# Kernel optimization log

Measured on AMD Instinct MI355X. Metric: run time of the kernel, lower is better.

Reference implementation:

```python
import jax, jax.numpy as jnp
import numpy as np
from jax import lax

NUM_CLASSES = 91
C_FEAT = 2048
HF = WF = 16          # backbone feature map size (512px image / stride 32)
STRIDE = 32           # anchor stride, as in source generate_base_anchors
N_ANCHOR_TYPES = 9
NMS_THR = 0.5
K_ROIS = 100          # fixed proposal count after NMS (padded, jit-safe)
SPATIAL_SCALE = 1.0 / 16.0
POOL = 7
SR = 2                # sampling ratio (source uses adaptive -1; fixed here)


def conv2d(x, w, b, pad):
    y = lax.conv_general_dilated(x, w, (1, 1), pad,
                                 dimension_numbers=('NCHW', 'OIHW', 'NCHW'))
    return y + b[None, :, None, None]


def setup_inputs():
    key = jax.random.key(0)
    ks = jax.random.split(key, 16)
    f32 = jnp.float32
    def w(k, shape, s=0.01):
        return jax.random.normal(k, shape, f32) * s
    z = lambda n: jnp.zeros((n,), f32)
    D = C_FEAT * POOL * POOL  # 100352
    return dict(
        x=jax.random.normal(ks[0], (1, C_FEAT, HF, WF), f32),
        rpn_w=w(ks[1], (512, C_FEAT, 3, 3)), rpn_b=z(512),
        cls_w=w(ks[2], (18, 512, 1, 1)), cls_b=z(18),
        bbox_w=w(ks[3], (36, 512, 1, 1)), bbox_b=z(36),
        fc1c_w=w(ks[4], (D, 4096)), fc1c_b=z(4096),
        fc2c_w=w(ks[5], (4096, NUM_CLASSES)), fc2c_b=z(NUM_CLASSES),
        fc1b_w=w(ks[6], (D, 4096)), fc1b_b=z(4096),
        fc2b_w=w(ks[7], (4096, 4)), fc2b_b=z(4),
        m1_w=w(ks[8], (256, C_FEAT, 3, 3)), m1_b=z(256),
        mt_w=w(ks[9], (256, 256, 2, 2)), mt_b=z(256),  # ConvT weight [C_in,C_out,kh,kw]
        m2_w=w(ks[10], (1, 256, 1, 1)), m2_b=z(1),
    )


def _anchors(hf, wf):
    scales = jnp.array([8.0, 16.0, 32.0])
    ratios = jnp.array([0.5, 1.0, 2.0])
    ws = (scales[:, None] * jnp.sqrt(ratios)[None, :]).reshape(-1)  # scale-major, 9
    hs = (scales[:, None] / jnp.sqrt(ratios)[None, :]).reshape(-1)
    base = jnp.stack([-ws / 2, -hs / 2, ws / 2, hs / 2], axis=1)    # [9,4]
    sy, sx = jnp.meshgrid(jnp.arange(hf) * STRIDE, jnp.arange(wf) * STRIDE, indexing='ij')
    shifts = jnp.stack([sx, sy, sx, sy], -1).reshape(-1, 4).astype(jnp.float32)  # [HW,4]
    return (base[:, None, :] + shifts[None, :, :]).reshape(-1, 4)   # [9*HW,4] anchor-type major


def _decode(a, d):
    wa = a[:, 2] - a[:, 0]
    ha = a[:, 3] - a[:, 1]
    cx = a[:, 0] + 0.5 * wa
    cy = a[:, 1] + 0.5 * ha
    px = cx + d[:, 0] * wa
    py = cy + d[:, 1] * ha
    pw = jnp.exp(d[:, 2]) * wa
    ph = jnp.exp(d[:, 3]) * ha
    return jnp.stack([px - 0.5 * pw, py - 0.5 * ph, px + 0.5 * pw, py + 0.5 * ph], 1)


def _nms_topk(boxes, scores, thr, k):
    n = boxes.shape[0]
    order = jnp.argsort(-scores)
    b = boxes[order]
    s = scores[order]
    area = (b[:, 2] - b[:, 0]) * (b[:, 3] - b[:, 1])
    xx1 = jnp.maximum(b[:, None, 0], b[None, :, 0])
    yy1 = jnp.maximum(b[:, None, 1], b[None, :, 1])
    xx2 = jnp.minimum(b[:, None, 2], b[None, :, 2])
    yy2 = jnp.minimum(b[:, None, 3], b[None, :, 3])
    inter = jnp.clip(xx2 - xx1, 0) * jnp.clip(yy2 - yy1, 0)
    iou = inter / (area[:, None] + area[None, :] - inter + 1e-9)
    j = jnp.arange(n)
    def body(i, keep):
        sup = keep[i] & (iou[i] > thr) & (j > i)
        return keep & ~sup
    keep = lax.fori_loop(0, n, body, jnp.ones((n,), bool))
    masked = jnp.where(keep, s, -jnp.inf)
    vals, pos = lax.top_k(masked, k)
    valid = jnp.isfinite(vals)
    fb = jnp.where(valid[:, None], b[pos], 0.0)
    fs = jnp.where(valid, vals, 0.0)
    return fb, fs


def _roi_align(feat, boxes):
    # feat: [C,H,W]; boxes: [K,4] in image coords
    C, H, W = feat.shape
    r = boxes * SPATIAL_SCALE
    S = POOL * SR  # 14 sample points per side
    t = (jnp.arange(S, dtype=feat.dtype) + 0.5) / S
    gx = jnp.clip(r[:, 0:1] + t[None, :] * (r[:, 2:3] - r[:, 0:1]), 0.0, W - 1.0)
    gy = jnp.clip(r[:, 1:2] + t[None, :] * (r[:, 3:4] - r[:, 1:2]), 0.0, H - 1.0)
    x0 = jnp.floor(gx); y0 = jnp.floor(gy)
    lx = gx - x0; ly = gy - y0
    x0i = x0.astype(jnp.int32); y0i = y0.astype(jnp.int32)
    x1i = jnp.minimum(x0i + 1, W - 1); y1i = jnp.minimum(y0i + 1, H - 1)
    flat = feat.reshape(C, H * W)
    def g(yi, xi):  # yi:[K,S] row coords, xi:[K,S] col coords -> [C,K,S,S]
        idx = yi[:, :, None] * W + xi[:, None, :]
        return flat[:, idx]
    lyb = ly[:, :, None]; lxb = lx[:, None, :]
    v = ((1 - lyb) * (1 - lxb) * g(y0i, x0i)
         + (1 - lyb) * lxb * g(y0i, x1i)
         + lyb * (1 - lxb) * g(y1i, x0i)
         + lyb * lxb * g(y1i, x1i))  # [C,K,S,S]
    v = v.reshape(C, -1, POOL, SR, POOL, SR).mean(axis=(3, 5))
    return v.transpose(1, 0, 2, 3)  # [K,C,7,7]


def reference(x, rpn_w, rpn_b, cls_w, cls_b, bbox_w, bbox_b,
              fc1c_w, fc1c_b, fc2c_w, fc2c_b,
              fc1b_w, fc1b_b, fc2b_w, fc2b_b,
              m1_w, m1_b, mt_w, mt_b, m2_w, m2_b):
    p1 = [(1, 1), (1, 1)]; p0 = [(0, 0), (0, 0)]
    f = jax.nn.relu(conv2d(x, rpn_w, rpn_b, p1))      # [1,512,H,W]
    obj = conv2d(f, cls_w, cls_b, p0)                 # [1,18,H,W]
    deltas = conv2d(f, bbox_w, bbox_b, p0)            # [1,36,H,W]
    hf, wf = f.shape[2], f.shape[3]
    hw = hf * wf
    # softmax over the 2 objectness classes (view(B,2,-1) layout)
    scores = jax.nn.softmax(obj.reshape(2, N_ANCHOR_TYPES, hw), axis=0)[1].reshape(-1)
    d = deltas.reshape(N_ANCHOR_TYPES, 4, hw).transpose(0, 2, 1).reshape(-1, 4)
    anchors = _anchors(hf, wf)
    boxes = _decode(anchors, d)
    fb, fs = _nms_topk(boxes, scores, NMS_THR, K_ROIS)
    rois = _roi_align(x[0], fb)                       # [K,2048,7,7]
    flat = rois.reshape(K_ROIS, -1)
    cls_out = jax.nn.relu(flat @ fc1c_w + fc1c_b) @ fc2c_w + fc2c_b
    box_out = jax.nn.relu(flat @ fc1b_w + fc1b_b) @ fc2b_w + fc2b_b
    m = jax.nn.relu(conv2d(rois, m1_w, m1_b, p1))     # [K,256,7,7]
    # ConvTranspose2d(k=2,s=2): non-overlapping, each pixel expands to a 2x2 block
    up = jnp.einsum('nchw,coij->nohiwj', m, mt_w).reshape(K_ROIS, 256, 2 * POOL, 2 * POOL)
    m = jax.nn.relu(up + mt_b[None, :, None, None])
    masks = conv2d(m, m2_w, m2_b, p0)                 # [K,1,14,14]
    return cls_out, box_out, masks
```

## Files before the change

### kernel.cpp

```cpp
#include <hip/hip_runtime.h>

#define DEVFN __device__ __forceinline__

typedef unsigned short ushort_t;
typedef unsigned int uint32;
typedef __attribute__((ext_vector_type(8))) short bf16x8;
typedef __attribute__((ext_vector_type(4))) float f32x4;

DEVFN ushort_t f2bf(float x) {
    uint32 b = __float_as_uint(x);
    uint32 r = (b + 0x7FFFu + ((b >> 16) & 1u)) >> 16;
    return (ushort_t)r;
}
DEVFN float bf2f(ushort_t u) { return __uint_as_float(((uint32)u) << 16); }

__global__ __launch_bounds__(256) void k_prep(const float* __restrict__ m1_w,
                                              const float* __restrict__ mt_w,
                                              const float* __restrict__ x,
                                              ushort_t* __restrict__ wAf,
                                              ushort_t* __restrict__ wA2f,
                                              float* __restrict__ xt) {
    const int bid = blockIdx.x, tid = threadIdx.x;
    if (bid < 256) {
        const int p = bid * 4 + (tid >> 6);
        const int lane = tid & 63, l15 = lane & 15, lg = lane >> 4;
        const int cot = p >> 6, cis = p & 63;
        const int co = cot * 16 + l15, k0 = cis * 32 + lg * 8;
        const float* src = m1_w + ((size_t)co * 2048 + k0) * 9;
        float v[72];
#pragma unroll
        for (int i = 0; i < 72; ++i) v[i] = src[i];
#pragma unroll
        for (int tap = 0; tap < 9; ++tap) {
            ushort_t* dst = wAf + ((size_t)((tap * 16 + cot) * 64 + cis) * 512) + lane * 8;
            ushort_t t8[8];
#pragma unroll
            for (int j = 0; j < 8; ++j) t8[j] = f2bf(v[j * 9 + tap]);
            uint4 u;
            u.x = (uint32)t8[0] | ((uint32)t8[1] << 16);
            u.y = (uint32)t8[2] | ((uint32)t8[3] << 16);
            u.z = (uint32)t8[4] | ((uint32)t8[5] << 16);
            u.w = (uint32)t8[6] | ((uint32)t8[7] << 16);
            *(uint4*)dst = u;
        }
    } else if (bid < 1280) {
        int idx = (bid - 256) * 256 + tid;
        int j = idx & 7, lane = (idx >> 3) & 63, cis = (idx >> 9) & 7, cot = idx >> 12;
        int row = cot * 16 + (lane & 15);
        int c = cis * 32 + (lane >> 4) * 8 + j;
        int o = row >> 2, ij = row & 3;
        wA2f[idx] = f2bf(mt_w[((size_t)c * 256 + o) * 4 + ij]);
    } else {
        int pos = bid - 1280;
        for (int i = 0; i < 8; ++i) {
            int c = tid + i * 256;
            xt[(size_t)pos * 2048 + c] = x[(size_t)c * 256 + pos];
        }
    }
}

__global__ __launch_bounds__(256) void k_rpn(const float* __restrict__ x,
                                             const float* __restrict__ rpn_w,
                                             float* __restrict__ fpart) {
    __shared__ float xs[8][18][18];
    const int coP = blockIdx.x, ks = blockIdx.y, tid = threadIdx.x;
    const int ty = tid >> 4, tx = tid & 15;
    const int co0 = coP * 4;
    for (int i = tid; i < 8 * 18 * 18; i += 256) ((float*)xs)[i] = 0.f;
    float acc[4] = {0.f, 0.f, 0.f, 0.f};
    for (int ch = 0; ch < 32; ++ch) {
        const int cib = ks * 256 + ch * 8;
        __syncthreads();
#pragma unroll
        for (int cc = 0; cc < 8; ++cc) xs[cc][ty + 1][tx + 1] = x[(size_t)(cib + cc) * 256 + tid];
        __syncthreads();
#pragma unroll
        for (int cc = 0; cc < 8; ++cc) {
            const int ci = cib + cc;
            float v[9];
#pragma unroll
            for (int t = 0; t < 9; ++t) v[t] = xs[cc][ty + t / 3][tx + t % 3];
            const float* wb = rpn_w + ((size_t)co0 * 2048 + ci) * 9;
#pragma unroll
            for (int o = 0; o < 4; ++o) {
                const float* w = wb + (size_t)o * 2048 * 9;
#pragma unroll
                for (int t = 0; t < 9; ++t) acc[o] = fmaf(v[t], w[t], acc[o]);
            }
        }
    }
#pragma unroll
    for (int o = 0; o < 4; ++o) fpart[((size_t)ks * 512 + co0 + o) * 256 + tid] = acc[o];
}

__global__ void k_rpn_reduce(const float* __restrict__ fpart, const float* __restrict__ rpn_b,
                             float* __restrict__ f) {
    const int i = blockIdx.x * 256 + threadIdx.x;
    float s = 0.f;
#pragma unroll
    for (int p = 0; p < 8; ++p) s += fpart[(size_t)p * 131072 + i];
    f[i] = fmaxf(s + rpn_b[i >> 8], 0.f);
}

__global__ void k_head(const float* __restrict__ f, const float* __restrict__ cls_w,
                       const float* __restrict__ cls_b, const float* __restrict__ bbox_w,
                       const float* __restrict__ bbox_b, float* __restrict__ scores,
                       float* __restrict__ boxes) {
    const int a = blockIdx.x, pos = threadIdx.x;
    float o0 = 0, o1 = 0, d0 = 0, d1 = 0, d2 = 0, d3 = 0;
    const float* c0 = cls_w + (size_t)a * 512;
    const float* c1 = cls_w + (size_t)(9 + a) * 512;
    const float* b0p = bbox_w + (size_t)(4 * a) * 512;
    const float* b1p = b0p + 512;
    const float* b2p = b0p + 1024;
    const float* b3p = b0p + 1536;
    for (int ci = 0; ci < 512; ++ci) {
        float fv = f[(size_t)ci * 256 + pos];
        o0 = fmaf(c0[ci], fv, o0);
        o1 = fmaf(c1[ci], fv, o1);
        d0 = fmaf(b0p[ci], fv, d0);
        d1 = fmaf(b1p[ci], fv, d1);
        d2 = fmaf(b2p[ci], fv, d2);
        d3 = fmaf(b3p[ci], fv, d3);
    }
    o0 += cls_b[a]; o1 += cls_b[9 + a];
    d0 += bbox_b[4 * a + 0]; d1 += bbox_b[4 * a + 1];
    d2 += bbox_b[4 * a + 2]; d3 += bbox_b[4 * a + 3];
    float mx = fmaxf(o0, o1);
    float e0 = expf(o0 - mx), e1 = expf(o1 - mx);
    float sc = e1 / (e0 + e1);
    int si = a / 3, ri = a % 3;
    float scale = (si == 0) ? 8.f : ((si == 1) ? 16.f : 32.f);
    float ratio = (ri == 0) ? 0.5f : ((ri == 1) ? 1.f : 2.f);
    float sq = sqrtf(ratio);
    float hw2 = (scale * sq) * 0.5f;
    float hh2 = (scale / sq) * 0.5f;
    int py = pos >> 4, px = pos & 15;
    float sx = (float)(px * 32), sy = (float)(py * 32);
    float a0 = sx - hw2, a1 = sy - hh2, a2 = sx + hw2, a3 = sy + hh2;
    float wa = a2 - a0, ha = a3 - a1;
    float cx = a0 + 0.5f * wa, cy = a1 + 0.5f * ha;
    float pxc = cx + d0 * wa, pyc = cy + d1 * ha;
    float pw = expf(d2) * wa, ph = expf(d3) * ha;
    int idx = a * 256 + pos;
    scores[idx] = sc;
    boxes[idx * 4 + 0] = pxc - 0.5f * pw;
    boxes[idx * 4 + 1] = pyc - 0.5f * ph;
    boxes[idx * 4 + 2] = pxc + 0.5f * pw;
    boxes[idx * 4 + 3] = pyc + 0.5f * ph;
}

__global__ void k_sort(const float* __restrict__ scores, const float* __restrict__ boxes,
                       float* __restrict__ ssort, float* __restrict__ bsort) {
    const int i = blockIdx.x * 256 + threadIdx.x;
    const float si = scores[i];
    int rank = 0;
    for (int j = 0; j < 2304; ++j) {
        float sj = scores[j];
        rank += (sj > si) || (sj == si && j < i);
    }
    ssort[rank] = si;
    float4 bb = *(const float4*)(boxes + (size_t)i * 4);
    *(float4*)(bsort + (size_t)rank * 4) = bb;
}

__global__ void k_adj(const float* __restrict__ bsort, unsigned long long* __restrict__ adj) {
    const int i = blockIdx.x, lane = threadIdx.x;
    const float4 bi = *(const float4*)(bsort + (size_t)i * 4);
    const float ai = (bi.z - bi.x) * (bi.w - bi.y);
    for (int w = 0; w < 36; ++w) {
        int j = w * 64 + lane;
        bool sup = false;
        if (j < 2304 && j > i) {
            float4 bj = *(const float4*)(bsort + (size_t)j * 4);
            float aj = (bj.z - bj.x) * (bj.w - bj.y);
            float xx1 = fmaxf(bi.x, bj.x), yy1 = fmaxf(bi.y, bj.y);
            float xx2 = fminf(bi.z, bj.z), yy2 = fminf(bi.w, bj.w);
            float inter = fmaxf(xx2 - xx1, 0.f) * fmaxf(yy2 - yy1, 0.f);
            float iou = inter / (ai + aj - inter + 1e-9f);
            sup = iou > 0.5f;
        }
        unsigned long long m = __ballot(sup);
        if (lane == 0) adj[(size_t)i * 36 + w] = m;
    }
}

__global__ void k_nms(const unsigned long long* __restrict__ adj, const float* __restrict__ bsort,
                      float* __restrict__ fb) {
    const int lane = threadIdx.x;
    unsigned long long r = (lane < 36) ? 0ULL : ~0ULL;
    int cnt = 0;
    for (int it = 0; it < 128; ++it) {
        unsigned long long inv = ~r;
        int local = inv ? (__ffsll((unsigned long long)inv) - 1) : 64;
        int cand = (local < 64) ? lane * 64 + local : (1 << 30);
#pragma unroll
        for (int d = 32; d; d >>= 1) cand = min(cand, __shfl_xor(cand, d));
        if (cand >= 2304) break;
        if (lane == 0) *(float4*)(fb + (size_t)cnt * 4) = *(const float4*)(bsort + (size_t)cand * 4);
        ++cnt;
        if (cnt == 100) break;
        unsigned long long a = (lane < 36) ? adj[(size_t)cand * 36 + lane] : 0ULL;
        r |= a;
        if (lane == (cand >> 6)) r |= 1ULL << (cand & 63);
    }
    for (int s2 = lane; s2 < 100; s2 += 64)
        if (s2 >= cnt) {
            float4 z = {0.f, 0.f, 0.f, 0.f};
            *(float4*)(fb + (size_t)s2 * 4) = z;
        }
}

__global__ __launch_bounds__(256) void k_roi(const float* __restrict__ xt,
                                             const float* __restrict__ fb,
                                             ushort_t* __restrict__ flatA,
                                             ushort_t* __restrict__ flatT) {
    __shared__ int sxi0[14], sxi1[14], syi0[14], syi1[14];
    __shared__ float slx[14], sly[14];
    const int cg = blockIdx.x, n = blockIdx.y, tid = threadIdx.x;
    const float r0 = fb[n * 4 + 0] * 0.0625f, r1 = fb[n * 4 + 1] * 0.0625f;
    const float r2 = fb[n * 4 + 2] * 0.0625f, r3 = fb[n * 4 + 3] * 0.0625f;
    if (tid < 14) {
        float tt = ((float)tid + 0.5f) * (1.0f / 14.0f);
        float gx = r0 + tt * (r2 - r0);
        gx = fminf(fmaxf(gx, 0.f), 15.f);
        float x0f = floorf(gx);
        int x0 = (int)x0f;
        sxi0[tid] = x0; sxi1[tid] = min(x0 + 1, 15); slx[tid] = gx - x0f;
        float gy = r1 + tt * (r3 - r1);
        gy = fminf(fmaxf(gy, 0.f), 15.f);
        float y0f = floorf(gy);
        int y0 = (int)y0f;
        syi0[tid] = y0; syi1[tid] = min(y0 + 1, 15); sly[tid] = gy - y0f;
    }
    __syncthreads();
    const int c = cg * 256 + tid;
    for (int py = 0; py < 7; ++py) {
        for (int px = 0; px < 7; ++px) {
            float accv = 0.f;
#pragma unroll
            for (int a2 = 0; a2 < 2; ++a2) {
                int sy = py * 2 + a2;
                int y0 = syi0[sy], y1 = syi1[sy];
                float ly = sly[sy];
#pragma unroll
                for (int b2 = 0; b2 < 2; ++b2) {
                    int sx = px * 2 + b2;
                    int x0 = sxi0[sx], x1 = sxi1[sx];
                    float lx = slx[sx];
                    float v00 = xt[(size_t)(y0 * 16 + x0) * 2048 + c];
                    float v01 = xt[(size_t)(y0 * 16 + x1) * 2048 + c];
                    float v10 = xt[(size_t)(y1 * 16 + x0) * 2048 + c];
                    float v11 = xt[(size_t)(y1 * 16 + x1) * 2048 + c];
                    accv += (1.f - ly) * (1.f - lx) * v00 + (1.f - ly) * lx * v01 +
                            ly * (1.f - lx) * v10 + ly * lx * v11;
                }
            }
            ushort_t bv = f2bf(accv * 0.25f);
            int pos = py * 7 + px;
            flatT[((size_t)n * 49 + pos) * 2048 + c] = bv;
            int k = c * 49 + pos;
            flatA[((size_t)(k >> 5) * 112 + n) * 32 + (k & 31)] = bv;
        }
    }
}

__global__ __launch_bounds__(256) void k_big(const ushort_t* __restrict__ flatA,
                                             const ushort_t* __restrict__ flatT,
                                             const float* __restrict__ Wc,
                                             const float* __restrict__ Wb,
                                             float* __restrict__ part,
                                             const ushort_t* __restrict__ wAf,
                                             const float* __restrict__ m1_b,
                                             ushort_t* __restrict__ m1outT) {
    const int bid = blockIdx.x, tid = threadIdx.x;
    const int wave = tid >> 6, lane = tid & 63, l15 = lane & 15, lg = lane >> 4;
    const f32x4 zz = {0.f, 0.f, 0.f, 0.f};
    if (bid < 77) {
        const int nb = bid;
        int nn[4], ppy[4], ppx[4], colv[4];
#pragma unroll
        for (int nt = 0; nt < 4; ++nt) {
            int col = nb * 64 + nt * 16 + l15;
            colv[nt] = col;
            int n = col / 49;
            int pos = col - n * 49;
            nn[nt] = n;
            ppy[nt] = pos / 7;
            ppx[nt] = pos - (pos / 7) * 7;
        }
        f32x4 acc[4][4];
#pragma unroll
        for (int a = 0; a < 4; ++a)
#pragma unroll
            for (int b = 0; b < 4; ++b) acc[a][b] = zz;
        bf16x8 zfrag;
#pragma unroll
        for (int j = 0; j < 8; ++j) zfrag[j] = 0;
        for (int tap = 0; tap < 9; ++tap) {
            const int ty = tap / 3 - 1, tx = tap % 3 - 1;
            int val[4];
            size_t bofs[4];
#pragma unroll
            for (int nt = 0; nt < 4; ++nt) {
                int iy = ppy[nt] + ty, ix = ppx[nt] + tx;
                val[nt] = (iy >= 0 && iy < 7 && ix >= 0 && ix < 7);
                bofs[nt] = ((size_t)nn[nt] * 49 + iy * 7 + ix) * 2048;
            }
            for (int cis = 0; cis < 64; ++cis) {
                const int kq = cis * 32 + lg * 8;
                bf16x8 a[4];
#pragma unroll
                for (int mt = 0; mt < 4; ++mt)
                    a[mt] = *(const bf16x8*)(wAf +
                            ((size_t)((tap * 16 + wave * 4 + mt) * 64 + cis) * 64 + lane) * 8);
                bf16x8 b[4];
#pragma unroll
                for (int nt = 0; nt < 4; ++nt)
                    b[nt] = val[nt] ? *(const bf16x8*)(flatT + bofs[nt] + kq) : zfrag;
#pragma unroll
                for (int nt = 0; nt < 4; ++nt)
#pragma unroll
                    for (int mt = 0; mt < 4; ++mt)
                        acc[mt][nt] = __builtin_amdgcn_mfma_f32_16x16x32_bf16(a[mt], b[nt], acc[mt][nt], 0, 0, 0);
            }
        }
#pragma unroll
        for (int mt = 0; mt < 4; ++mt)
#pragma unroll
            for (int nt = 0; nt < 4; ++nt) {
                int co0 = wave * 64 + mt * 16 + lg * 4;
                ushort_t v[4];
#pragma unroll
                for (int r = 0; r < 4; ++r)
                    v[r] = f2bf(fmaxf(acc[mt][nt][r] + m1_b[co0 + r], 0.f));
                uint2 u;
                u.x = (uint32)v[0] | ((uint32)v[1] << 16);
                u.y = (uint32)v[2] | ((uint32)v[3] << 16);
                *(uint2*)(m1outT + (size_t)colv[nt] * 256 + co0) = u;
            }
        return;
    }
    const int b = bid - 77;
    const int x = b & 7, i = b >> 3;
    const int nb = i & 31;
    const int g = x + 8 * (i >> 5);
    const int kc = g >> 1, br = g & 1;
    const float* W = br ? Wb : Wc;
    const int ncol0 = nb * 128 + wave * 32;
    const size_t wstep = (size_t)32 * 4096;
    const float* wp = W + ((size_t)kc * 196 * 32 + lg * 8) * 4096 + ncol0 + l15;
    const ushort_t* ap = flatA + ((size_t)kc * 196 * 112 + l15) * 32 + lg * 8;
    float wc[16], wn[16];
#pragma unroll
    for (int j = 0; j < 8; ++j) {
        wc[j] = wp[(size_t)j * 4096];
        wc[8 + j] = wp[(size_t)j * 4096 + 16];
    }
    f32x4 acc0[7], acc1[7];
#pragma unroll
    for (int t = 0; t < 7; ++t) { acc0[t] = zz; acc1[t] = zz; }
    for (int s = 0; s < 196; s += 2) {
        const float* wp1 = wp + wstep;
#pragma unroll
        for (int j = 0; j < 8; ++j) {
            wn[j] = wp1[(size_t)j * 4096];
            wn[8 + j] = wp1[(size_t)j * 4096 + 16];
        }
        bf16x8 af[7];
#pragma unroll
        for (int t = 0; t < 7; ++t) af[t] = *(const bf16x8*)(ap + (size_t)t * 512);
        bf16x8 b0, b1;
#pragma unroll
        for (int j = 0; j < 8; ++j) {
            b0[j] = (short)f2bf(wc[j]);
            b1[j] = (short)f2bf(wc[8 + j]);
        }
#pragma unroll
        for (int t = 0; t < 7; ++t) {
            acc0[t] = __builtin_amdgcn_mfma_f32_16x16x32_bf16(af[t], b0, acc0[t], 0, 0, 0);
            acc1[t] = __builtin_amdgcn_mfma_f32_16x16x32_bf16(af[t], b1, acc1[t], 0, 0, 0);
        }
        const float* wp2 = (s + 2 < 196) ? wp + 2 * wstep : wp;
#pragma unroll
        for (int j = 0; j < 8; ++j) {
            wc[j] = wp2[(size_t)j * 4096];
            wc[8 + j] = wp2[(size_t)j * 4096 + 16];
        }
        bf16x8 af2[7];
#pragma unroll
        for (int t = 0; t < 7; ++t) af2[t] = *(const bf16x8*)(ap + 3584 + (size_t)t * 512);
#pragma unroll
        for (int j = 0; j < 8; ++j) {
            b0[j] = (short)f2bf(wn[j]);
            b1[j] = (short)f2bf(wn[8 + j]);
        }
#pragma unroll
        for (int t = 0; t < 7; ++t) {
            acc0[t] = __builtin_amdgcn_mfma_f32_16x16x32_bf16(af2[t], b0, acc0[t], 0, 0, 0);
            acc1[t] = __builtin_amdgcn_mfma_f32_16x16x32_bf16(af2[t], b1, acc1[t], 0, 0, 0);
        }
        wp += 2 * wstep;
        ap += 2 * 3584;
    }
    float* pb = part + (size_t)(br * 16 + kc) * 112 * 4096;
#pragma unroll
    for (int t = 0; t < 7; ++t)
#pragma unroll
        for (int r = 0; r < 4; ++r) {
            int m = t * 16 + lg * 4 + r;
            pb[(size_t)m * 4096 + ncol0 + l15] = acc0[t][r];
            pb[(size_t)m * 4096 + ncol0 + 16 + l15] = acc1[t][r];
        }
}

__global__ __launch_bounds__(256) void k_fc2(const float* __restrict__ part,
                                             const float* __restrict__ fc1c_b,
                                             const float* __restrict__ fc1b_b,
                                             const float* __restrict__ Wc,
                                             const float* __restrict__ bc,
                                             const float* __restrict__ Wb,
                                             const float* __restrict__ bb,
                                             float* __restrict__ out) {
    __shared__ float h_s[2][4096];
    const int m = blockIdx.x, tid = threadIdx.x;
    for (int i = tid; i < 8192; i += 256) {
        int br = i >> 12, col = i & 4095;
        float s = br ? fc1b_b[col] : fc1c_b[col];
#pragma unroll
        for (int p = 0; p < 16; ++p) s += part[((size_t)(br * 16 + p) * 112 + m) * 4096 + col];
        h_s[br][col] = fmaxf(s, 0.f);
    }
    __syncthreads();
    if (tid < 91) {
        float acc = bc[tid];
        for (int k = 0; k < 4096; ++k) acc = fmaf(h_s[0][k], Wc[(size_t)k * 91 + tid], acc);
        out[m * 91 + tid] = acc;
    } else if (tid >= 96 && tid < 100) {
        int col = tid - 96;
        float acc = bb[col];
        for (int k = 0; k < 4096; ++k) acc = fmaf(h_s[1][k], Wb[(size_t)k * 4 + col], acc);
        out[9100 + m * 4 + col] = acc;
    }
}

__global__ __launch_bounds__(256) void k_up(const ushort_t* __restrict__ m1outT,
                                            const ushort_t* __restrict__ wA2f,
                                            ushort_t* __restrict__ upT) {
    const int nb = blockIdx.x, cq = blockIdx.y, tid = threadIdx.x;
    const int wave = tid >> 6, lane = tid & 63, l15 = lane & 15, lg = lane >> 4;
    int colv[4];
#pragma unroll
    for (int nt = 0; nt < 4; ++nt) colv[nt] = nb * 64 + nt * 16 + l15;
    f32x4 acc[4][4];
    const f32x4 zz = {0.f, 0.f, 0.f, 0.f};
#pragma unroll
    for (int a = 0; a < 4; ++a)
#pragma unroll
        for (int b = 0; b < 4; ++b) acc[a][b] = zz;
    for (int cis = 0; cis < 8; ++cis) {
        const int kq = cis * 32 + lg * 8;
        bf16x8 a[4];
#pragma unroll
        for (int mt = 0; mt < 4; ++mt)
            a[mt] = *(const bf16x8*)(wA2f +
                    ((size_t)((cq * 16 + wave * 4 + mt) * 8 + cis) * 64 + lane) * 8);
        bf16x8 b[4];
#pragma unroll
        for (int nt = 0; nt < 4; ++nt)
            b[nt] = *(const bf16x8*)(m1outT + (size_t)colv[nt] * 256 + kq);
#pragma unroll
        for (int nt = 0; nt < 4; ++nt)
#pragma unroll
            for (int mt = 0; mt < 4; ++mt)
                acc[mt][nt] = __builtin_amdgcn_mfma_f32_16x16x32_bf16(a[mt], b[nt], acc[mt][nt], 0, 0, 0);
    }
#pragma unroll
    for (int mt = 0; mt < 4; ++mt)
#pragma unroll
        for (int nt = 0; nt < 4; ++nt) {
            int rb = (cq * 16 + wave * 4 + mt) * 16 + lg * 4;
            ushort_t v[4];
#pragma unroll
            for (int r = 0; r < 4; ++r) v[r] = f2bf(acc[mt][nt][r]);
            uint2 u;
            u.x = (uint32)v[0] | ((uint32)v[1] << 16);
            u.y = (uint32)v[2] | ((uint32)v[3] << 16);
            *(uint2*)(upT + (size_t)colv[nt] * 1024 + rb) = u;
        }
}

__global__ void k_mask(const ushort_t* __restrict__ upT, const float* __restrict__ mt_b,
                       const float* __restrict__ m2_w, const float* __restrict__ m2_b,
                       float* __restrict__ out) {
    const int n = blockIdx.x, t = threadIdx.x;
    if (t >= 196) return;
    const int ys = t / 14, xs = t % 14;
    const int ro = (ys & 1) * 2 + (xs & 1);
    const int col = n * 49 + (ys >> 1) * 7 + (xs >> 1);
    float acc = m2_b[0];
    for (int o = 0; o < 256; ++o) {
        float v = bf2f(upT[(size_t)col * 1024 + o * 4 + ro]) + mt_b[o];
        v = fmaxf(v, 0.f);
        acc = fmaf(m2_w[o], v, acc);
    }
    out[9500 + n * 196 + t] = acc;
}

extern "C" void kernel_launch(void* const* d_in, const int* in_sizes, int n_in,
                              void* d_out, int out_size, void* d_ws, size_t ws_size,
                              hipStream_t stream) {
    const float* x      = (const float*)d_in[0];
    const float* rpn_w  = (const float*)d_in[1];
    const float* rpn_b  = (const float*)d_in[2];
    const float* cls_w  = (const float*)d_in[3];
    const float* cls_b  = (const float*)d_in[4];
    const float* bbox_w = (const float*)d_in[5];
    const float* bbox_b = (const float*)d_in[6];
    const float* fc1c_w = (const float*)d_in[7];
    const float* fc1c_b = (const float*)d_in[8];
    const float* fc2c_w = (const float*)d_in[9];
    const float* fc2c_b = (const float*)d_in[10];
    const float* fc1b_w = (const float*)d_in[11];
    const float* fc1b_b = (const float*)d_in[12];
    const float* fc2b_w = (const float*)d_in[13];
    const float* fc2b_b = (const float*)d_in[14];
    const float* m1_w   = (const float*)d_in[15];
    const float* m1_b   = (const float*)d_in[16];
    const float* mt_w   = (const float*)d_in[17];
    const float* mt_b   = (const float*)d_in[18];
    const float* m2_w   = (const float*)d_in[19];
    const float* m2_b   = (const float*)d_in[20];
    float* out = (float*)d_out;

    char* ws = (char*)d_ws;
    size_t off = 0;
    auto take = [&](size_t nbytes) -> char* {
        char* p = ws + off;
        off += (nbytes + 255) & ~(size_t)255;
        return p;
    };
    float* xt      = (float*)take(2097152);
    float* fpart   = (float*)take(4194304);
    float* f       = (float*)take(524288);
    float* scores  = (float*)take(9216);
    float* boxes   = (float*)take(36864);
    float* ssort   = (float*)take(9216);
    float* bsort   = (float*)take(36864);
    unsigned long long* adj = (unsigned long long*)take(663552);
    float* fb      = (float*)take(1600);
    ushort_t* flatA = (ushort_t*)take(22478848);
    ushort_t* flatT = (ushort_t*)take(20471808);
    float* part1   = (float*)take(58720256);
    ushort_t* wAf  = (ushort_t*)take(9437184);
    ushort_t* m1outT = (ushort_t*)take(2523136);
    ushort_t* wA2f = (ushort_t*)take(524288);
    ushort_t* upT  = (ushort_t*)part1;

    k_prep<<<1536, 256, 0, stream>>>(m1_w, mt_w, x, wAf, wA2f, xt);
    k_rpn<<<dim3(128, 8), 256, 0, stream>>>(x, rpn_w, fpart);
    k_rpn_reduce<<<512, 256, 0, stream>>>(fpart, rpn_b, f);
    k_head<<<9, 256, 0, stream>>>(f, cls_w, cls_b, bbox_w, bbox_b, scores, boxes);
    k_sort<<<9, 256, 0, stream>>>(scores, boxes, ssort, bsort);
    k_adj<<<2304, 64, 0, stream>>>(bsort, adj);
    k_nms<<<1, 64, 0, stream>>>(adj, bsort, fb);
    k_roi<<<dim3(8, 100), 256, 0, stream>>>(xt, fb, flatA, flatT);
    k_big<<<1101, 256, 0, stream>>>(flatA, flatT, fc1c_w, fc1b_w, part1, wAf, m1_b, m1outT);
    k_fc2<<<100, 256, 0, stream>>>(part1, fc1c_b, fc1b_b, fc2c_w, fc2c_b, fc2b_w, fc2b_b, out);
    k_up<<<dim3(77, 4), 256, 0, stream>>>(m1outT, wA2f, upT);
    k_mask<<<100, 256, 0, stream>>>(upT, mt_b, m2_w, m2_b, out);
}
```

Before: 1.686 ms.

## Stage FC weights through LDS with async loads and split small-head reductions

The big FC GEMM now streams fp32 weight tiles into double-buffered LDS with global_load_lds, converts them with packed bf16 conversion instructions, and uses a new block-to-tile mapping with a min-occupancy launch bound. The fc2 head splits its K reduction across two thread halves with multiple accumulators. The RPN head and mask kernels are unrolled with independent accumulators for more ILP. The aim is better memory latency hiding on the weight stream, which dominates the runtime, at the cost of two barriers per K step and extra LDS pressure.

Result: faster. 1.491 ms (-11.6%).

```diff
diff --git a/kernel.cpp b/kernel.cpp
--- a/kernel.cpp
+++ b/kernel.cpp
@@ -7,12 +7,17 @@
 typedef __attribute__((ext_vector_type(8))) short bf16x8;
 typedef __attribute__((ext_vector_type(4))) float f32x4;
 
+typedef __attribute__((address_space(3))) unsigned int lds_uint;
+typedef const __attribute__((address_space(1))) unsigned int glob_uint;
+
 DEVFN ushort_t f2bf(float x) {
     uint32 b = __float_as_uint(x);
     uint32 r = (b + 0x7FFFu + ((b >> 16) & 1u)) >> 16;
     return (ushort_t)r;
 }
 DEVFN float bf2f(ushort_t u) { return __uint_as_float(((uint32)u) << 16); }
+
+union BWU { uint32 u[4]; bf16x8 v8; };
 
 __global__ __launch_bounds__(256) void k_prep(const float* __restrict__ m1_w,
                                               const float* __restrict__ mt_w,
@@ -114,14 +119,19 @@
     const float* b1p = b0p + 512;
     const float* b2p = b0p + 1024;
     const float* b3p = b0p + 1536;
-    for (int ci = 0; ci < 512; ++ci) {
-        float fv = f[(size_t)ci * 256 + pos];
-        o0 = fmaf(c0[ci], fv, o0);
-        o1 = fmaf(c1[ci], fv, o1);
-        d0 = fmaf(b0p[ci], fv, d0);
-        d1 = fmaf(b1p[ci], fv, d1);
-        d2 = fmaf(b2p[ci], fv, d2);
-        d3 = fmaf(b3p[ci], fv, d3);
+    for (int ci = 0; ci < 512; ci += 8) {
+        float fv[8];
+#pragma unroll
+        for (int j = 0; j < 8; ++j) fv[j] = f[(size_t)(ci + j) * 256 + pos];
+#pragma unroll
+        for (int j = 0; j < 8; ++j) {
+            o0 = fmaf(c0[ci + j], fv[j], o0);
+            o1 = fmaf(c1[ci + j], fv[j], o1);
+            d0 = fmaf(b0p[ci + j], fv[j], d0);
+            d1 = fmaf(b1p[ci + j], fv[j], d1);
+            d2 = fmaf(b2p[ci + j], fv[j], d2);
+            d3 = fmaf(b3p[ci + j], fv[j], d3);
+        }
     }
     o0 += cls_b[a]; o1 += cls_b[9 + a];
     d0 += bbox_b[4 * a + 0]; d1 += bbox_b[4 * a + 1];
@@ -265,14 +275,15 @@
     }
 }
 
-__global__ __launch_bounds__(256) void k_big(const ushort_t* __restrict__ flatA,
-                                             const ushort_t* __restrict__ flatT,
-                                             const float* __restrict__ Wc,
-                                             const float* __restrict__ Wb,
-                                             float* __restrict__ part,
-                                             const ushort_t* __restrict__ wAf,
-                                             const float* __restrict__ m1_b,
-                                             ushort_t* __restrict__ m1outT) {
+__global__ __launch_bounds__(256, 4) void k_big(const ushort_t* __restrict__ flatA,
+                                                const ushort_t* __restrict__ flatT,
+                                                const float* __restrict__ Wc,
+                                                const float* __restrict__ Wb,
+                                                float* __restrict__ part,
+                                                const ushort_t* __restrict__ wAf,
+                                                const float* __restrict__ m1_b,
+                                                ushort_t* __restrict__ m1outT) {
+    __shared__ float wlds[2][32][128];
     const int bid = blockIdx.x, tid = threadIdx.x;
     const int wave = tid >> 6, lane = tid & 63, l15 = lane & 15, lg = lane >> 4;
     const f32x4 zz = {0.f, 0.f, 0.f, 0.f};
@@ -341,76 +352,64 @@
             }
         return;
     }
-    const int b = bid - 77;
-    const int x = b & 7, i = b >> 3;
-    const int nb = i & 31;
-    const int g = x + 8 * (i >> 5);
-    const int kc = g >> 1, br = g & 1;
+    const int h = bid - 77;
+    const int x = h & 7, t = h >> 3;
+    const int colTile = t >> 2, rem = t & 3;
+    const int kc = x * 2 + (rem & 1), br = rem >> 1;
     const float* W = br ? Wb : Wc;
-    const int ncol0 = nb * 128 + wave * 32;
-    const size_t wstep = (size_t)32 * 4096;
-    const float* wp = W + ((size_t)kc * 196 * 32 + lg * 8) * 4096 + ncol0 + l15;
-    const ushort_t* ap = flatA + ((size_t)kc * 196 * 112 + l15) * 32 + lg * 8;
-    float wc[16], wn[16];
-#pragma unroll
-    for (int j = 0; j < 8; ++j) {
-        wc[j] = wp[(size_t)j * 4096];
-        wc[8 + j] = wp[(size_t)j * 4096 + 16];
-    }
+    const int ncol0 = colTile * 128 + wave * 32;
+    const int k0 = kc * 6272;
+    const float* wbase = W + (size_t)k0 * 4096 + colTile * 128;
+    const int srow = lane >> 5, scol = (lane & 31) * 4;
+
+    auto stage = [&](int buf, int s) {
+        const float* g0 = wbase + ((size_t)(s * 32 + wave * 8 + srow)) * 4096 + scol;
+#pragma unroll
+        for (int q = 0; q < 4; ++q) {
+            const float* g = g0 + (size_t)(q * 2) * 4096;
+            float* l = &wlds[buf][wave * 8 + q * 2][0];
+            __builtin_amdgcn_global_load_lds((glob_uint*)g, (lds_uint*)l, 16, 0, 0);
+        }
+    };
+
     f32x4 acc0[7], acc1[7];
 #pragma unroll
-    for (int t = 0; t < 7; ++t) { acc0[t] = zz; acc1[t] = zz; }
-    for (int s = 0; s < 196; s += 2) {
-        const float* wp1 = wp + wstep;
-#pragma unroll
-        for (int j = 0; j < 8; ++j) {
-            wn[j] = wp1[(size_t)j * 4096];
-            wn[8 + j] = wp1[(size_t)j * 4096 + 16];
-        }
+    for (int tt = 0; tt < 7; ++tt) { acc0[tt] = zz; acc1[tt] = zz; }
+
+    stage(0, 0);
+    const ushort_t* ap = flatA + ((size_t)(kc * 196) * 112 + l15) * 32 + lg * 8;
+    for (int s = 0; s < 196; ++s) {
+        const int b = s & 1;
+        if (s + 1 < 196) stage(b ^ 1, s + 1);
         bf16x8 af[7];
 #pragma unroll
-        for (int t = 0; t < 7; ++t) af[t] = *(const bf16x8*)(ap + (size_t)t * 512);
-        bf16x8 b0, b1;
-#pragma unroll
-        for (int j = 0; j < 8; ++j) {
-            b0[j] = (short)f2bf(wc[j]);
-            b1[j] = (short)f2bf(wc[8 + j]);
-        }
-#pragma unroll
-        for (int t = 0; t < 7; ++t) {
-            acc0[t] = __builtin_amdgcn_mfma_f32_16x16x32_bf16(af[t], b0, acc0[t], 0, 0, 0);
-            acc1[t] = __builtin_amdgcn_mfma_f32_16x16x32_bf16(af[t], b1, acc1[t], 0, 0, 0);
-        }
-        const float* wp2 = (s + 2 < 196) ? wp + 2 * wstep : wp;
-#pragma unroll
-        for (int j = 0; j < 8; ++j) {
-            wc[j] = wp2[(size_t)j * 4096];
-            wc[8 + j] = wp2[(size_t)j * 4096 + 16];
-        }
-        bf16x8 af2[7];
-#pragma unroll
-        for (int t = 0; t < 7; ++t) af2[t] = *(const bf16x8*)(ap + 3584 + (size_t)t * 512);
-#pragma unroll
-        for (int j = 0; j < 8; ++j) {
-            b0[j] = (short)f2bf(wn[j]);
-            b1[j] = (short)f2bf(wn[8 + j]);
-        }
-#pragma unroll
-        for (int t = 0; t < 7; ++t) {
-            acc0[t] = __builtin_amdgcn_mfma_f32_16x16x32_bf16(af2[t], b0, acc0[t], 0, 0, 0);
-            acc1[t] = __builtin_amdgcn_mfma_f32_16x16x32_bf16(af2[t], b1, acc1[t], 0, 0, 0);
-        }
-        wp += 2 * wstep;
-        ap += 2 * 3584;
+        for (int tt = 0; tt < 7; ++tt) af[tt] = *(const bf16x8*)(ap + (size_t)tt * 512);
+        __syncthreads();
+        const float* wrow = &wlds[b][lg * 8][wave * 32 + l15];
+        BWU b0u, b1u;
+#pragma unroll
+        for (int i = 0; i < 4; ++i) {
+            float w0a = wrow[(2 * i) * 128], w0b = wrow[(2 * i + 1) * 128];
+            float w1a = wrow[(2 * i) * 128 + 16], w1b = wrow[(2 * i + 1) * 128 + 16];
+            asm("v_cvt_pk_bf16_f32 %0, %1, %2" : "=v"(b0u.u[i]) : "v"(w0a), "v"(w0b));
+            asm("v_cvt_pk_bf16_f32 %0, %1, %2" : "=v"(b1u.u[i]) : "v"(w1a), "v"(w1b));
+        }
+#pragma unroll
+        for (int tt = 0; tt < 7; ++tt) {
+            acc0[tt] = __builtin_amdgcn_mfma_f32_16x16x32_bf16(af[tt], b0u.v8, acc0[tt], 0, 0, 0);
+            acc1[tt] = __builtin_amdgcn_mfma_f32_16x16x32_bf16(af[tt], b1u.v8, acc1[tt], 0, 0, 0);
+        }
+        __syncthreads();
+        ap += 3584;
     }
     float* pb = part + (size_t)(br * 16 + kc) * 112 * 4096;
 #pragma unroll
-    for (int t = 0; t < 7; ++t)
+    for (int tt = 0; tt < 7; ++tt)
 #pragma unroll
         for (int r = 0; r < 4; ++r) {
-            int m = t * 16 + lg * 4 + r;
-            pb[(size_t)m * 4096 + ncol0 + l15] = acc0[t][r];
-            pb[(size_t)m * 4096 + ncol0 + 16 + l15] = acc1[t][r];
+            int m = tt * 16 + lg * 4 + r;
+            pb[(size_t)m * 4096 + ncol0 + l15] = acc0[tt][r];
+            pb[(size_t)m * 4096 + ncol0 + 16 + l15] = acc1[tt][r];
         }
 }
 
@@ -423,6 +422,8 @@
                                              const float* __restrict__ bb,
                                              float* __restrict__ out) {
     __shared__ float h_s[2][4096];
+    __shared__ float ph[2][91];
+    __shared__ float pbx[2][4];
     const int m = blockIdx.x, tid = threadIdx.x;
     for (int i = tid; i < 8192; i += 256) {
         int br = i >> 12, col = i & 4095;
@@ -432,15 +433,44 @@
         h_s[br][col] = fmaxf(s, 0.f);
     }
     __syncthreads();
-    if (tid < 91) {
-        float acc = bc[tid];
-        for (int k = 0; k < 4096; ++k) acc = fmaf(h_s[0][k], Wc[(size_t)k * 91 + tid], acc);
-        out[m * 91 + tid] = acc;
-    } else if (tid >= 96 && tid < 100) {
-        int col = tid - 96;
-        float acc = bb[col];
-        for (int k = 0; k < 4096; ++k) acc = fmaf(h_s[1][k], Wb[(size_t)k * 4 + col], acc);
-        out[9100 + m * 4 + col] = acc;
+    const int half = tid >> 7, col = tid & 127;
+    if (col < 91) {
+        const float* hrow = &h_s[0][half * 2048];
+        const float* wp = Wc + (size_t)half * 2048 * 91 + col;
+        float a0 = 0, a1 = 0, a2 = 0, a3 = 0, a4 = 0, a5 = 0, a6 = 0, a7 = 0;
+        for (int k = 0; k < 2048; k += 8) {
+            a0 = fmaf(hrow[k],     wp[(size_t)k * 91], a0);
+            a1 = fmaf(hrow[k + 1], wp[(size_t)(k + 1) * 91], a1);
+            a2 = fmaf(hrow[k + 2], wp[(size_t)(k + 2) * 91], a2);
+            a3 = fmaf(hrow[k + 3], wp[(size_t)(k + 3) * 91], a3);
+            a4 = fmaf(hrow[k + 4], wp[(size_t)(k + 4) * 91], a4);
+            a5 = fmaf(hrow[k + 5], wp[(size_t)(k + 5) * 91], a5);
+            a6 = fmaf(hrow[k + 6], wp[(size_t)(k + 6) * 91], a6);
+            a7 = fmaf(hrow[k + 7], wp[(size_t)(k + 7) * 91], a7);
+        }
+        ph[half][col] = ((a0 + a1) + (a2 + a3)) + ((a4 + a5) + (a6 + a7));
+    } else if (col >= 96 && col < 100) {
+        int bcol = col - 96;
+        const float* hrow = &h_s[1][half * 2048];
+        const float* wp = Wb + (size_t)half * 2048 * 4 + bcol;
+        float a0 = 0, a1 = 0, a2 = 0, a3 = 0, a4 = 0, a5 = 0, a6 = 0, a7 = 0;
+        for (int k = 0; k < 2048; k += 8) {
+            a0 = fmaf(hrow[k],     wp[(size_t)k * 4], a0);
+            a1 = fmaf(hrow[k + 1], wp[(size_t)(k + 1) * 4], a1);
+            a2 = fmaf(hrow[k + 2], wp[(size_t)(k + 2) * 4], a2);
+            a3 = fmaf(hrow[k + 3], wp[(size_t)(k + 3) * 4], a3);
+            a4 = fmaf(hrow[k + 4], wp[(size_t)(k + 4) * 4], a4);
+            a5 = fmaf(hrow[k + 5], wp[(size_t)(k + 5) * 4], a5);
+            a6 = fmaf(hrow[k + 6], wp[(size_t)(k + 6) * 4], a6);
+            a7 = fmaf(hrow[k + 7], wp[(size_t)(k + 7) * 4], a7);
+        }
+        pbx[half][bcol] = ((a0 + a1) + (a2 + a3)) + ((a4 + a5) + (a6 + a7));
+    }
+    __syncthreads();
+    if (tid < 91) out[m * 91 + tid] = bc[tid] + ph[0][tid] + ph[1][tid];
+    else if (tid >= 96 && tid < 100) {
+        int bcol = tid - 96;
+        out[9100 + m * 4 + bcol] = bb[bcol] + pbx[0][bcol] + pbx[1][bcol];
     }
 }
 
@@ -498,13 +528,16 @@
     const int ys = t / 14, xs = t % 14;
     const int ro = (ys & 1) * 2 + (xs & 1);
     const int col = n * 49 + (ys >> 1) * 7 + (xs >> 1);
-    float acc = m2_b[0];
-    for (int o = 0; o < 256; ++o) {
-        float v = bf2f(upT[(size_t)col * 1024 + o * 4 + ro]) + mt_b[o];
-        v = fmaxf(v, 0.f);
-        acc = fmaf(m2_w[o], v, acc);
-    }
-    out[9500 + n * 196 + t] = acc;
+    const ushort_t* up0 = upT + (size_t)col * 1024 + ro;
+    float a0 = m2_b[0], a1 = 0.f, a2 = 0.f, a3 = 0.f;
+#pragma unroll 4
+    for (int o = 0; o < 256; o += 4) {
+        a0 = fmaf(m2_w[o],     fmaxf(bf2f(up0[(o) * 4]) + mt_b[o], 0.f), a0);
+        a1 = fmaf(m2_w[o + 1], fmaxf(bf2f(up0[(o + 1) * 4]) + mt_b[o + 1], 0.f), a1);
+        a2 = fmaf(m2_w[o + 2], fmaxf(bf2f(up0[(o + 2) * 4]) + mt_b[o + 2], 0.f), a2);
+        a3 = fmaf(m2_w[o + 3], fmaxf(bf2f(up0[(o + 3) * 4]) + mt_b[o + 3], 0.f), a3);
+    }
+    out[9500 + n * 196 + t] = (a0 + a1) + (a2 + a3);
 }
 
 extern "C" void kernel_launch(void* const* d_in, const int* in_sizes, int n_in,
```
